# Performance work log

Hardware: AMD Instinct MI355X
Metric: run time of the kernel (lower is better)

The kernel has to match this reference:

```python
import jax, jax.numpy as jnp
import numpy as np

N_HEADS = 4
T_OUT = 24  # total T; y has T - t_in steps


def setup_inputs() -> dict:
    key = jax.random.key(0)
    k1, k2, k3, k4 = jax.random.split(key, 4)
    B, t_in, N, C, K = 2, 12, 10000, 16, 17  # K = k + 1 (self)
    x = jax.random.normal(k1, (B, t_in, N, C), dtype=jnp.float32)
    nearest_nodes = jax.random.randint(k2, (N, K), 0, N, dtype=jnp.int32)
    nearest_dists = jax.random.uniform(k3, (N, K), dtype=jnp.float32)
    shrink_w = jax.random.normal(k4, (T_OUT - t_in, t_in * N_HEADS), dtype=jnp.float32) * 0.1
    shrink_b = jnp.zeros((T_OUT - t_in,), dtype=jnp.float32)
    return {"x": x, "nearest_nodes": nearest_nodes, "nearest_dists": nearest_dists,
            "shrink_w": shrink_w, "shrink_b": shrink_b}


def reference(x, nearest_nodes, nearest_dists, shrink_w, shrink_b):
    B, t_in, N, C = x.shape
    H = N_HEADS
    # sigma = nearest_dists.max() / sigma_ratio, with sigma_ratio = 1
    sigma = jnp.max(nearest_dists)
    lam = jnp.arange(1, H + 1, dtype=x.dtype) / H  # (H,)
    # distance weights per head: (N, K, H)
    w = jnp.exp(-(nearest_dists[..., None] ** 2) * lam / (sigma ** 2))
    w = jnp.where((nearest_nodes == -1)[..., None], 0.0, w)
    w = jnp.where(w < 1e-8, 0.0, w)
    # pad node at index N; -1 neighbors map to pad (weight already zero)
    pad_x = jnp.concatenate([x, jnp.zeros_like(x[:, :, :1])], axis=2)  # (B,T,N+1,C)
    idx = jnp.where(nearest_nodes == -1, N, nearest_nodes)  # (N, K)
    g = pad_x[:, :, idx]  # (B, t_in, N, K, C) neighbor gather
    # weighted reduce over neighbor axis -> (B, t_in, N, H, C)
    agg = jnp.einsum('btnkc,nkh->btnhc', g, w)
    # (B, N, C, t_in*H)
    a = jnp.transpose(agg, (0, 2, 4, 1, 3)).reshape(B, N, C, t_in * H)
    y = a @ shrink_w.T + shrink_b  # (B, N, C, T - t_in)
    y = jnp.transpose(y, (0, 3, 1, 2))  # (B, T - t_in, N, C)
    y = jax.nn.selu(y)  # CustomActivationFunction default mode='selu'
    return jnp.concatenate([x, y], axis=1)  # (B, T, N, C)
```

## Files before the change

kernel.cpp:

```cpp
#include <hip/hip_runtime.h>
#include <hip/hip_bf16.h>
#include <math.h>

#define NB      2
#define T_IN    12
#define T_OUT_  24
#define O_OUT   12
#define NN      10000
#define CC      16
#define KK      17
#define HH      4
#define JJ      48
#define PL      24
#define TN      64
#define TBLK    157
#define SBLK    167
#define GN      8
#define GBLK    1250
#define PSTR    68
#define ANS     (PL * PSTR)

__device__ __forceinline__ unsigned int f2bf(float f) {
    union { float f; unsigned int u; } v; v.f = f;
    unsigned int r = v.u + 0x7FFFu + ((v.u >> 16) & 1u);
    return r >> 16;
}
__device__ __forceinline__ float bf2f(unsigned int lo16) {
    union { unsigned int u; float f; } v; v.u = lo16 << 16;
    return v.f;
}

__global__ __launch_bounds__(256) void setup_kernel(
    const float* __restrict__ x,
    const float* __restrict__ dists, int ndists,
    float* __restrict__ out,
    unsigned short* __restrict__ xt,
    int* __restrict__ sigma_bits)
{
    const int tid = threadIdx.x;
    if (blockIdx.x < TBLK) {
        const int n0 = blockIdx.x * TN;
        const int q  = tid & 3;
        const int nl = tid >> 2;
        const int n  = n0 + nl;
        if (n < NN) {
            uint2* xtp = (uint2*)xt + n * (PL * 4) + q;
            #pragma unroll
            for (int p = 0; p < PL; ++p) {
                const float4 v = *(const float4*)(x + (p * NN + n) * CC + q * 4);
                const int b = p / T_IN, t = p % T_IN;
                *(float4*)(out + ((b * T_OUT_ + t) * NN + n) * CC + q * 4) = v;
                uint2 pk;
                pk.x = f2bf(v.x) | (f2bf(v.y) << 16);
                pk.y = f2bf(v.z) | (f2bf(v.w) << 16);
                xtp[p * 4] = pk;
            }
        }
    } else {
        const int sb = blockIdx.x - TBLK;
        float m = 0.0f;
        const int nv4 = ndists >> 2;
        const float4* d4 = (const float4*)dists;
        for (int i = sb * 256 + tid; i < nv4; i += SBLK * 256) {
            float4 v = d4[i];
            m = fmaxf(fmaxf(m, fmaxf(v.x, v.y)), fmaxf(v.z, v.w));
        }
        for (int i = (nv4 << 2) + sb * 256 + tid; i < ndists; i += SBLK * 256)
            m = fmaxf(m, dists[i]);
        #pragma unroll
        for (int off = 32; off > 0; off >>= 1)
            m = fmaxf(m, __shfl_down(m, off, 64));
        __shared__ float sm[4];
        int lane = tid & 63, wid = tid >> 6;
        if (lane == 0) sm[wid] = m;
        __syncthreads();
        if (tid == 0) {
            float mm = fmaxf(fmaxf(sm[0], sm[1]), fmaxf(sm[2], sm[3]));
            atomicMax(sigma_bits, __float_as_int(mm));
        }
    }
}

__global__ __launch_bounds__(384) void fused_kernel(
    const unsigned short* __restrict__ xt,
    const int*   __restrict__ nodes,
    const float* __restrict__ dists,
    const int*   __restrict__ sigma_bits,
    const float* __restrict__ Wm,
    const float* __restrict__ bias,
    float* __restrict__ out)
{
    const int tid = threadIdx.x;
    const int n0  = blockIdx.x * GN;

    __shared__ int   lidx[GN * KK];
    __shared__ float lw[GN * KK][HH];
    __shared__ float W_s[O_OUT * JJ];
    __shared__ float b_s[O_OUT];
    __shared__ float a_s[4 * ANS];

    for (int i = tid; i < O_OUT * JJ; i += 384) W_s[i] = Wm[i];
    if (tid < O_OUT) b_s[tid] = bias[tid];

    const float sigma  = __int_as_float(*sigma_bits);
    const float inv_s2 = 1.0f / (sigma * sigma);
    if (tid < GN * KK) {
        const int   nd = nodes[n0 * KK + tid];
        const float dd = dists[n0 * KK + tid];
        const float e1 = expf(-dd * dd * inv_s2 * 0.25f);
        float w0 = e1, w1 = e1 * e1, w2 = w1 * e1, w3 = w1 * w1;
        if (nd == -1) { w0 = w1 = w2 = w3 = 0.f; }
        if (w0 < 1e-8f) w0 = 0.f;
        if (w1 < 1e-8f) w1 = 0.f;
        if (w2 < 1e-8f) w2 = 0.f;
        if (w3 < 1e-8f) w3 = 0.f;
        lidx[tid]  = ((nd < 0) ? 0 : nd) * (PL * CC * 2);
        lw[tid][0] = w0; lw[tid][1] = w1; lw[tid][2] = w2; lw[tid][3] = w3;
    }
    __syncthreads();

    const int slot = tid / 96;
    const int l96  = tid % 96;

    const float kScale = 1.0507009873554805f;
    const float kAlpha = 1.6732632423543772f;

    for (int g = 0; g < GN / 4; ++g) {
        const int nl = g * 4 + slot;
        const int rb = nl * KK;

        float4 ah0 = {0,0,0,0}, ah1 = {0,0,0,0}, ah2 = {0,0,0,0}, ah3 = {0,0,0,0};
        #pragma unroll
        for (int k = 0; k < KK; ++k) {
            const uint2 gv = *(const uint2*)((const char*)xt + lidx[rb + k] + l96 * 8);
            const float g0 = bf2f(gv.x & 0xffffu), g1 = bf2f(gv.x >> 16);
            const float g2 = bf2f(gv.y & 0xffffu), g3 = bf2f(gv.y >> 16);
            const float w0 = lw[rb + k][0], w1 = lw[rb + k][1];
            const float w2 = lw[rb + k][2], w3 = lw[rb + k][3];
            ah0.x += g0 * w0; ah0.y += g1 * w0; ah0.z += g2 * w0; ah0.w += g3 * w0;
            ah1.x += g0 * w1; ah1.y += g1 * w1; ah1.z += g2 * w1; ah1.w += g3 * w1;
            ah2.x += g0 * w2; ah2.y += g1 * w2; ah2.z += g2 * w2; ah2.w += g3 * w2;
            ah3.x += g0 * w3; ah3.y += g1 * w3; ah3.z += g2 * w3; ah3.w += g3 * w3;
        }

        __syncthreads();
        {
            const int q = l96 & 3, plane = l96 >> 2;
            float* ap = a_s + slot * ANS + plane * PSTR + q * 16;
            *(float4*)(ap + 0)  = make_float4(ah0.x, ah1.x, ah2.x, ah3.x);
            *(float4*)(ap + 4)  = make_float4(ah0.y, ah1.y, ah2.y, ah3.y);
            *(float4*)(ap + 8)  = make_float4(ah0.z, ah1.z, ah2.z, ah3.z);
            *(float4*)(ap + 12) = make_float4(ah0.w, ah1.w, ah2.w, ah3.w);
        }
        __syncthreads();

        #pragma unroll
        for (int j = 0; j < 4; ++j) {
            const int oid = tid + 384 * j;
            const int c   = oid & 15;
            const int r   = oid >> 4;
            const int o   = r % O_OUT;
            const int rr  = r / O_OUT;
            const int b   = rr & 1;
            const int ns  = rr >> 1;
            const float* abase = a_s + ns * ANS + b * (T_IN * PSTR) + c * 4;
            const float* wbase = W_s + o * JJ;
            float y = b_s[o];
            #pragma unroll
            for (int t = 0; t < T_IN; ++t) {
                const float4 av = *(const float4*)(abase + t * PSTR);
                const float4 wv = *(const float4*)(wbase + t * 4);
                y += av.x * wv.x + av.y * wv.y + av.z * wv.z + av.w * wv.w;
            }
            y = (y > 0.0f) ? kScale * y : kScale * kAlpha * expm1f(y);
            const int n = n0 + g * 4 + ns;
            out[((b * T_OUT_ + T_IN + o) * NN + n) * CC + c] = y;
        }
    }
}

extern "C" void kernel_launch(void* const* d_in, const int* in_sizes, int n_in,
                              void* d_out, int out_size, void* d_ws, size_t ws_size,
                              hipStream_t stream) {
    const float* x     = (const float*)d_in[0];
    const int*   nodes = (const int*)  d_in[1];
    const float* dists = (const float*)d_in[2];
    const float* Wm    = (const float*)d_in[3];
    const float* bias  = (const float*)d_in[4];
    float* out = (float*)d_out;

    char* ws = (char*)d_ws;
    int*            sigma_bits = (int*)ws;
    unsigned short* xt         = (unsigned short*)(ws + 1024);

    const int ndists = in_sizes[2];
    setup_kernel<<<TBLK + SBLK, 256, 0, stream>>>(x, dists, ndists, out, xt,
                                                  sigma_bits);
    fused_kernel<<<GBLK, 384, 0, stream>>>(xt, nodes, dists, sigma_bits,
                                           Wm, bias, out);
}
```

Measured before the change: 117.8 us.

## Widen gather to 16B loads, process all 8 nodes at once, bf16 staging

The setup kernel now copies and transposes x in per-timestep chunks across many more blocks, giving contiguous reads in place of strided per-node ones. The fused kernel assigns 48 threads per node so all 8 nodes gather together with 16-byte loads. This removes the two-iteration loop and its extra barriers. The aggregated activations are stored to shared memory as packed bf16, halving LDS footprint and traffic, at the cost of extra rounding before the output projection.

```diff
diff --git a/kernel.cpp b/kernel.cpp
--- a/kernel.cpp
+++ b/kernel.cpp
@@ -12,22 +12,25 @@
 #define HH      4
 #define JJ      48
 #define PL      24
-#define TN      64
-#define TBLK    157
+#define XCHN    40
+#define CHN     250
+#define XBLK    (PL * XCHN)
 #define SBLK    167
 #define GN      8
-#define GBLK    1250
-#define PSTR    68
-#define ANS     (PL * PSTR)
+#define GBLK    (NN / GN)
+#define PSTRU   34
+#define ANSU    (PL * PSTRU)
 
 __device__ __forceinline__ unsigned int f2bf(float f) {
     union { float f; unsigned int u; } v; v.f = f;
     unsigned int r = v.u + 0x7FFFu + ((v.u >> 16) & 1u);
     return r >> 16;
 }
-__device__ __forceinline__ float bf2f(unsigned int lo16) {
-    union { unsigned int u; float f; } v; v.u = lo16 << 16;
-    return v.f;
+__device__ __forceinline__ float bf_lo(unsigned int u) {
+    union { unsigned int u; float f; } v; v.u = u << 16; return v.f;
+}
+__device__ __forceinline__ float bf_hi(unsigned int u) {
+    union { unsigned int u; float f; } v; v.u = u & 0xffff0000u; return v.f;
 }
 
 __global__ __launch_bounds__(256) void setup_kernel(
@@ -38,26 +41,25 @@
     int* __restrict__ sigma_bits)
 {
     const int tid = threadIdx.x;
-    if (blockIdx.x < TBLK) {
-        const int n0 = blockIdx.x * TN;
-        const int q  = tid & 3;
-        const int nl = tid >> 2;
-        const int n  = n0 + nl;
-        if (n < NN) {
-            uint2* xtp = (uint2*)xt + n * (PL * 4) + q;
-            #pragma unroll
-            for (int p = 0; p < PL; ++p) {
-                const float4 v = *(const float4*)(x + (p * NN + n) * CC + q * 4);
-                const int b = p / T_IN, t = p % T_IN;
-                *(float4*)(out + ((b * T_OUT_ + t) * NN + n) * CC + q * 4) = v;
-                uint2 pk;
-                pk.x = f2bf(v.x) | (f2bf(v.y) << 16);
-                pk.y = f2bf(v.z) | (f2bf(v.w) << 16);
-                xtp[p * 4] = pk;
-            }
+    if (blockIdx.x < XBLK) {
+        const int p  = blockIdx.x / XCHN;
+        const int ch = blockIdx.x % XCHN;
+        const int b = p / T_IN, t = p % T_IN;
+        const int n0 = ch * CHN;
+        const float* xp = x + (long)(p * NN + n0) * CC;
+        float* op = out + (long)((b * T_OUT_ + t) * NN + n0) * CC;
+        uint2* xtp = (uint2*)xt + (long)n0 * (PL * 4) + p * 4;
+        for (int i = tid; i < CHN * 4; i += 256) {
+            const int nl = i >> 2, q = i & 3;
+            const float4 v = *(const float4*)(xp + i * 4);
+            *(float4*)(op + i * 4) = v;
+            uint2 pk;
+            pk.x = f2bf(v.x) | (f2bf(v.y) << 16);
+            pk.y = f2bf(v.z) | (f2bf(v.w) << 16);
+            xtp[(long)nl * (PL * 4) + q] = pk;
         }
     } else {
-        const int sb = blockIdx.x - TBLK;
+        const int sb = blockIdx.x - XBLK;
         float m = 0.0f;
         const int nv4 = ndists >> 2;
         const float4* d4 = (const float4*)dists;
@@ -93,11 +95,11 @@
     const int tid = threadIdx.x;
     const int n0  = blockIdx.x * GN;
 
-    __shared__ int   lidx[GN * KK];
-    __shared__ float lw[GN * KK][HH];
-    __shared__ float W_s[O_OUT * JJ];
-    __shared__ float b_s[O_OUT];
-    __shared__ float a_s[4 * ANS];
+    __shared__ int      lidx[GN * KK];
+    __shared__ float    lw[GN * KK][HH];
+    __shared__ float    W_s[O_OUT * JJ];
+    __shared__ float    b_s[O_OUT];
+    __shared__ unsigned a_s[GN * ANSU];
 
     for (int i = tid; i < O_OUT * JJ; i += 384) W_s[i] = Wm[i];
     if (tid < O_OUT) b_s[tid] = bias[tid];
@@ -119,63 +121,73 @@
     }
     __syncthreads();
 
-    const int slot = tid / 96;
-    const int l96  = tid % 96;
+    const int slot  = tid / 48;
+    const int l     = tid % 48;
+    const int rb    = slot * KK;
+    const int plane = l >> 1;
+    const int co    = (l & 1) * 8;
+    const char* xtb = (const char*)xt;
+
+    float acc[HH][8];
+    #pragma unroll
+    for (int h = 0; h < HH; ++h)
+        #pragma unroll
+        for (int j = 0; j < 8; ++j) acc[h][j] = 0.f;
+
+    #pragma unroll
+    for (int k = 0; k < KK; ++k) {
+        const uint4  gv = *(const uint4*)(xtb + lidx[rb + k] + (l << 4));
+        const float4 wv = *(const float4*)lw[rb + k];
+        float g[8];
+        g[0] = bf_lo(gv.x); g[1] = bf_hi(gv.x);
+        g[2] = bf_lo(gv.y); g[3] = bf_hi(gv.y);
+        g[4] = bf_lo(gv.z); g[5] = bf_hi(gv.z);
+        g[6] = bf_lo(gv.w); g[7] = bf_hi(gv.w);
+        #pragma unroll
+        for (int j = 0; j < 8; ++j) {
+            acc[0][j] += g[j] * wv.x;
+            acc[1][j] += g[j] * wv.y;
+            acc[2][j] += g[j] * wv.z;
+            acc[3][j] += g[j] * wv.w;
+        }
+    }
+
+    {
+        unsigned* ap = a_s + slot * ANSU + plane * PSTRU + co * 2;
+        #pragma unroll
+        for (int j = 0; j < 8; ++j) {
+            uint2 pk;
+            pk.x = f2bf(acc[0][j]) | (f2bf(acc[1][j]) << 16);
+            pk.y = f2bf(acc[2][j]) | (f2bf(acc[3][j]) << 16);
+            *(uint2*)(ap + j * 2) = pk;
+        }
+    }
+    __syncthreads();
 
     const float kScale = 1.0507009873554805f;
     const float kAlpha = 1.6732632423543772f;
-
-    for (int g = 0; g < GN / 4; ++g) {
-        const int nl = g * 4 + slot;
-        const int rb = nl * KK;
-
-        float4 ah0 = {0,0,0,0}, ah1 = {0,0,0,0}, ah2 = {0,0,0,0}, ah3 = {0,0,0,0};
-        #pragma unroll
-        for (int k = 0; k < KK; ++k) {
-            const uint2 gv = *(const uint2*)((const char*)xt + lidx[rb + k] + l96 * 8);
-            const float g0 = bf2f(gv.x & 0xffffu), g1 = bf2f(gv.x >> 16);
-            const float g2 = bf2f(gv.y & 0xffffu), g3 = bf2f(gv.y >> 16);
-            const float w0 = lw[rb + k][0], w1 = lw[rb + k][1];
-            const float w2 = lw[rb + k][2], w3 = lw[rb + k][3];
-            ah0.x += g0 * w0; ah0.y += g1 * w0; ah0.z += g2 * w0; ah0.w += g3 * w0;
-            ah1.x += g0 * w1; ah1.y += g1 * w1; ah1.z += g2 * w1; ah1.w += g3 * w1;
-            ah2.x += g0 * w2; ah2.y += g1 * w2; ah2.z += g2 * w2; ah2.w += g3 * w2;
-            ah3.x += g0 * w3; ah3.y += g1 * w3; ah3.z += g2 * w3; ah3.w += g3 * w3;
-        }
-
-        __syncthreads();
-        {
-            const int q = l96 & 3, plane = l96 >> 2;
-            float* ap = a_s + slot * ANS + plane * PSTR + q * 16;
-            *(float4*)(ap + 0)  = make_float4(ah0.x, ah1.x, ah2.x, ah3.x);
-            *(float4*)(ap + 4)  = make_float4(ah0.y, ah1.y, ah2.y, ah3.y);
-            *(float4*)(ap + 8)  = make_float4(ah0.z, ah1.z, ah2.z, ah3.z);
-            *(float4*)(ap + 12) = make_float4(ah0.w, ah1.w, ah2.w, ah3.w);
-        }
-        __syncthreads();
-
-        #pragma unroll
-        for (int j = 0; j < 4; ++j) {
-            const int oid = tid + 384 * j;
-            const int c   = oid & 15;
-            const int r   = oid >> 4;
-            const int o   = r % O_OUT;
-            const int rr  = r / O_OUT;
-            const int b   = rr & 1;
-            const int ns  = rr >> 1;
-            const float* abase = a_s + ns * ANS + b * (T_IN * PSTR) + c * 4;
-            const float* wbase = W_s + o * JJ;
-            float y = b_s[o];
-            #pragma unroll
-            for (int t = 0; t < T_IN; ++t) {
-                const float4 av = *(const float4*)(abase + t * PSTR);
-                const float4 wv = *(const float4*)(wbase + t * 4);
-                y += av.x * wv.x + av.y * wv.y + av.z * wv.z + av.w * wv.w;
-            }
-            y = (y > 0.0f) ? kScale * y : kScale * kAlpha * expm1f(y);
-            const int n = n0 + g * 4 + ns;
-            out[((b * T_OUT_ + T_IN + o) * NN + n) * CC + c] = y;
-        }
+    #pragma unroll
+    for (int jj = 0; jj < 8; ++jj) {
+        const int oid = tid + 384 * jj;
+        const int c   = oid & 15;
+        const int r   = oid >> 4;
+        const int o   = r % O_OUT;
+        const int rr  = r / O_OUT;
+        const int b   = rr & 1;
+        const int ns  = rr >> 1;
+        const unsigned* abase = a_s + ns * ANSU + (b * T_IN) * PSTRU + c * 2;
+        const float*    wb    = W_s + o * JJ;
+        float y = b_s[o];
+        #pragma unroll
+        for (int t = 0; t < T_IN; ++t) {
+            const uint2 av = *(const uint2*)(abase + t * PSTRU);
+            y += bf_lo(av.x) * wb[t * 4 + 0];
+            y += bf_hi(av.x) * wb[t * 4 + 1];
+            y += bf_lo(av.y) * wb[t * 4 + 2];
+            y += bf_hi(av.y) * wb[t * 4 + 3];
+        }
+        y = (y > 0.0f) ? kScale * y : kScale * kAlpha * expm1f(y);
+        out[((long)(b * T_OUT_ + T_IN + o) * NN + n0 + ns) * CC + c] = y;
     }
 }
 
@@ -194,7 +206,7 @@
     unsigned short* xt         = (unsigned short*)(ws + 1024);
 
     const int ndists = in_sizes[2];
-    setup_kernel<<<TBLK + SBLK, 256, 0, stream>>>(x, dists, ndists, out, xt,
+    setup_kernel<<<XBLK + SBLK, 256, 0, stream>>>(x, dists, ndists, out, xt,
                                                   sigma_bits);
     fused_kernel<<<GBLK, 384, 0, stream>>>(xt, nodes, dists, sigma_bits,
                                            Wm, bias, out);
```

Result: slower. 121.9 us (+3.5%).
